# Kernel optimization log

Hardware: AMD Instinct MI355X
Metric: run time of the kernel (lower is better)

Reference implementation:

```python
import jax, jax.numpy as jnp
import numpy as np
import math

D_MODEL = 32
N_HEADS = 2
FEAT_DIM = 16
HEAD_DIM = 16  # d_model // num_key_value_heads
EPS = 1e-12
R2 = math.sqrt(2.0)
RD = math.sqrt(FEAT_DIM)
RRD = math.sqrt(RD)


def taylor_exp(x):
    # x: (b, h, l, f) -> (b, h, l, 1 + f + f*f)
    b, h, l, f = x.shape
    x2 = (x[..., :, None] * x[..., None, :]).reshape(b, h, l, f * f) / R2
    term1 = jnp.ones_like(x[..., :1])
    term2 = x / RRD
    term3 = x2 / RD
    return jnp.concatenate([term1, term2, term3], axis=-1)


def setup_inputs() -> dict:
    key = jax.random.key(0)
    ks = jax.random.split(key, 5)
    b, l = 4, 2048
    return {
        "hidden_states": jax.random.normal(ks[0], (b, l, D_MODEL), dtype=jnp.float32),
        "Wq": jax.random.normal(ks[1], (FEAT_DIM * N_HEADS, D_MODEL), dtype=jnp.float32) * (1.0 / math.sqrt(D_MODEL)),
        "Wk": jax.random.normal(ks[2], (FEAT_DIM * N_HEADS, D_MODEL), dtype=jnp.float32) * (1.0 / math.sqrt(D_MODEL)),
        "Wv": jax.random.normal(ks[3], (N_HEADS * HEAD_DIM, D_MODEL), dtype=jnp.float32) * (1.0 / math.sqrt(D_MODEL)),
        "Wo": jax.random.normal(ks[4], (D_MODEL, N_HEADS * HEAD_DIM), dtype=jnp.float32) * (1.0 / math.sqrt(D_MODEL)),
    }


def reference(hidden_states, Wq, Wk, Wv, Wo):
    b, l, _ = hidden_states.shape
    # projections (nn.Linear: x @ W.T)
    q = (hidden_states @ Wq.T).reshape(b, l, N_HEADS, FEAT_DIM).transpose(0, 2, 1, 3)  # (b,h,l,f)
    k = (hidden_states @ Wk.T).reshape(b, l, N_HEADS, FEAT_DIM).transpose(0, 2, 1, 3)
    v = (hidden_states @ Wv.T).reshape(b, l, N_HEADS, HEAD_DIM).transpose(0, 2, 1, 3)  # (b,h,l,d)

    q = taylor_exp(q)  # (b,h,l,D) with D = 1+f+f^2 = 273
    k = taylor_exp(k)

    # causal linear attention: num_t = q_t . sum_{s<=t} k_s v_s^T
    kv = jnp.cumsum(k[..., None, :] * v[..., :, None], axis=2)  # (b,h,l,d,D)
    num = jnp.einsum('bhlD,bhldD->bhld', q, kv)                  # (b,h,l,d)
    denom = jnp.einsum('bhlD,bhlD->bhl', q, jnp.cumsum(k, axis=2)) + EPS
    y = num / denom[..., None]

    y = y.transpose(0, 2, 1, 3).reshape(b, l, N_HEADS * HEAD_DIM)  # (b,l,h*d)
    return (y @ Wo.T).astype(hidden_states.dtype)
```

## Files before the change

kernel.cpp:

```cpp
#include <hip/hip_runtime.h>
#include <math.h>

#define B 4
#define H 2
#define L 2048
#define DM 32
#define F 16
#define HD 16
#define DD 273
#define CHK 64
#define NC (L / CHK)
#define BH (B * H)

#define SC_LIN 0.5f
#define SC_QUAD 0.17677669529663687f

__global__ __launch_bounds__(256) void proj_kernel(
    const float* __restrict__ hs, const float* __restrict__ Wq,
    const float* __restrict__ Wk, const float* __restrict__ Wv,
    float* __restrict__ qp, float* __restrict__ kp, float* __restrict__ vp) {
  int lane = threadIdx.x & 63;
  int wave = __builtin_amdgcn_readfirstlane(threadIdx.x >> 6);
  int rg = blockIdx.x >> 1;
  int half = blockIdx.x & 1;
  int row = rg * 64 + lane;
  int b = row >> 11, l = row & (L - 1);

  float x[DM];
  const float4* xr = (const float4*)(hs + (size_t)row * DM);
#pragma unroll
  for (int j = 0; j < DM / 4; j++) {
    float4 v = xr[j];
    x[4 * j] = v.x; x[4 * j + 1] = v.y; x[4 * j + 2] = v.z; x[4 * j + 3] = v.w;
  }
  int c0 = half * 48 + wave * 12;
  for (int c = c0; c < c0 + 12; c++) {
    int kind = c >> 5;
    int cc = c & 31;
    const float* __restrict__ W = (kind == 0) ? Wq : (kind == 1) ? Wk : Wv;
    const float* __restrict__ wr = W + (size_t)cc * DM;
    float acc = 0.f;
#pragma unroll
    for (int i = 0; i < DM; i++) acc += x[i] * wr[i];
    int h = cc >> 4, f = cc & 15;
    float* dst = (kind == 0) ? qp : (kind == 1) ? kp : vp;
    dst[(((size_t)(b * H + h) * L) + l) * F + f] = acc;
  }
}

__global__ __launch_bounds__(256) void chunksum_kernel(
    const float* __restrict__ kp, const float* __restrict__ vp,
    float* __restrict__ S_kv, float* __restrict__ S_k) {
  int blk = blockIdx.x;
  int bh = blk >> 5, ch = blk & (NC - 1);
  __shared__ float ks[CHK][F + 1];

  const float4* kb = (const float4*)(kp + ((size_t)bh * L + (size_t)ch * CHK) * F);
  {
    int r = threadIdx.x >> 2, c4 = (threadIdx.x & 3) * 4;
    float4 v = kb[threadIdx.x];
    ks[r][c4] = v.x; ks[r][c4 + 1] = v.y; ks[r][c4 + 2] = v.z; ks[r][c4 + 3] = v.w;
  }
  if (threadIdx.x < CHK) ks[threadIdx.x][16] = 1.0f;
  __syncthreads();

  const float* __restrict__ vbase = vp + ((size_t)bh * L + (size_t)ch * CHK) * F;

#pragma unroll
  for (int rep = 0; rep < 2; rep++) {
    int dd = threadIdx.x + rep * 256;
    if (dd >= DD) break;
    int i, j;
    float sc;
    if (dd == 0) {
      i = 16; j = 16; sc = 1.0f;
    } else if (dd <= F) {
      i = dd - 1; j = 16; sc = SC_LIN;
    } else {
      int m = dd - 17;
      i = m >> 4; j = m & 15; sc = SC_QUAD;
    }
    float acc[HD];
#pragma unroll
    for (int hh = 0; hh < HD; hh++) acc[hh] = 0.f;
    float acck = 0.f;
    for (int p = 0; p < CHK; p++) {
      float kf = sc * ks[p][i] * ks[p][j];
      acck += kf;
      const float* __restrict__ vr = vbase + p * F;
#pragma unroll
      for (int hh = 0; hh < HD; hh++) acc[hh] += kf * vr[hh];
    }
    float* dst = S_kv + ((size_t)blk * DD + dd) * HD;
#pragma unroll
    for (int hh = 0; hh < HD; hh++) dst[hh] = acc[hh];
    S_k[(size_t)blk * DD + dd] = acck;
  }
}

#define PSLICES 19
__global__ __launch_bounds__(256) void prefix_kernel(float* __restrict__ S_kv,
                                                     float* __restrict__ S_k) {
  int blk = blockIdx.x;
  int bh = blk / PSLICES, sl = blk % PSLICES;
  int e = sl * 256 + threadIdx.x;
  if (e < DD * HD) {
    size_t base = (size_t)bh * NC * DD * HD + e;
    float v[NC];
#pragma unroll
    for (int c = 0; c < NC; c++) v[c] = S_kv[base + (size_t)c * DD * HD];
    float run = 0.f;
#pragma unroll
    for (int c = 0; c < NC; c++) {
      S_kv[base + (size_t)c * DD * HD] = run;
      run += v[c];
    }
  } else if (e < DD * HD + DD) {
    int e2 = e - DD * HD;
    size_t base = (size_t)bh * NC * DD + e2;
    float v[NC];
#pragma unroll
    for (int c = 0; c < NC; c++) v[c] = S_k[base + (size_t)c * DD];
    float run = 0.f;
#pragma unroll
    for (int c = 0; c < NC; c++) {
      S_k[base + (size_t)c * DD] = run;
      run += v[c];
    }
  }
}

__global__ __launch_bounds__(512) void outchunk_kernel(
    const float* __restrict__ qp, const float* __restrict__ kp,
    const float* __restrict__ vp, const float* __restrict__ St_kv,
    const float* __restrict__ St_k, float* __restrict__ y) {
  int blk = blockIdx.x;
  int bh = blk >> 5, ch = blk & (NC - 1);
  int b = bh >> 1, h = bh & 1;
  int t = threadIdx.x & 63;
  int u = __builtin_amdgcn_readfirstlane(threadIdx.x >> 6);

  __shared__ float qs[CHK][F + 1];
  __shared__ float red[8][CHK][21];

  if (threadIdx.x < 256) {
    const float4* qb =
        (const float4*)(qp + ((size_t)bh * L + (size_t)ch * CHK) * F);
    int r = threadIdx.x >> 2, c4 = (threadIdx.x & 3) * 4;
    float4 v = qb[threadIdx.x];
    qs[r][c4] = v.x; qs[r][c4 + 1] = v.y; qs[r][c4 + 2] = v.z; qs[r][c4 + 3] = v.w;
    if (threadIdx.x < CHK) qs[threadIdx.x][16] = 1.0f;
  }

  float qreg[F];
  const float4* qrow =
      (const float4*)(qp + ((size_t)bh * L + (size_t)ch * CHK + t) * F);
#pragma unroll
  for (int j = 0; j < 4; j++) {
    float4 v = qrow[j];
    qreg[4 * j] = v.x; qreg[4 * j + 1] = v.y;
    qreg[4 * j + 2] = v.z; qreg[4 * j + 3] = v.w;
  }
  __syncthreads();

  float acc[HD];
#pragma unroll
  for (int hh = 0; hh < HD; hh++) acc[hh] = 0.f;
  float den = 0.f;

  const float* __restrict__ Sbase = St_kv + (size_t)blk * DD * HD;
  const float* __restrict__ Skb = St_k + (size_t)blk * DD;

  for (int m = 0; m < 35; m++) {
    int dd = u + (m << 3);
    if (dd >= DD) break;
    float phi;
    if (dd == 0) {
      phi = 1.0f;
    } else if (dd <= F) {
      phi = qs[t][dd - 1] * SC_LIN;
    } else {
      int mm = dd - 17;
      phi = qs[t][mm >> 4] * qs[t][mm & 15] * SC_QUAD;
    }
    den += phi * Skb[dd];
    const float* __restrict__ Sr = Sbase + dd * HD;
#pragma unroll
    for (int jj = 0; jj < HD; jj++) acc[jj] += phi * Sr[jj];
  }

  const float* __restrict__ kbase = kp + ((size_t)bh * L + (size_t)ch * CHK) * F;
  const float* __restrict__ vbase = vp + ((size_t)bh * L + (size_t)ch * CHK) * F;
#pragma unroll
  for (int mm = 0; mm < CHK / 8; mm++) {
    int s = u + mm * 8;
    const float* __restrict__ kr = kbase + s * F;
    float dot = 0.f;
#pragma unroll
    for (int i = 0; i < F; i++) dot += qreg[i] * kr[i];
    float scv = 1.0f + dot * 0.25f + dot * dot * 0.03125f;
    scv = (s <= t) ? scv : 0.0f;
    den += scv;
    const float* __restrict__ vr = vbase + s * F;
#pragma unroll
    for (int hh = 0; hh < HD; hh++) acc[hh] += scv * vr[hh];
  }

#pragma unroll
  for (int hh = 0; hh < HD; hh++) red[u][t][hh] = acc[hh];
  red[u][t][16] = den;
  __syncthreads();

  for (int idx = threadIdx.x; idx < CHK * 17; idx += 512) {
    int t2 = idx / 17, e = idx % 17;
    float sum = 0.f;
#pragma unroll
    for (int w = 0; w < 8; w++) sum += red[w][t2][e];
    red[0][t2][e] = sum;
  }
  __syncthreads();

  if (threadIdx.x < CHK) {
    int t2 = threadIdx.x;
    float inv = 1.0f / (red[0][t2][16] + 1e-12f);
    float* yb = y + (((size_t)(b * L + ch * CHK + t2)) * H + h) * HD;
#pragma unroll
    for (int hh = 0; hh < HD; hh++) yb[hh] = red[0][t2][hh] * inv;
  }
}

__global__ __launch_bounds__(256) void out_kernel(const float* __restrict__ y,
                                                  const float* __restrict__ Wo,
                                                  float* __restrict__ out) {
  int lane = threadIdx.x & 63;
  int wave = __builtin_amdgcn_readfirstlane(threadIdx.x >> 6);
  int row = blockIdx.x * 64 + lane;
  float yr[DM];
  const float4* yb = (const float4*)(y + (size_t)row * DM);
#pragma unroll
  for (int j = 0; j < DM / 4; j++) {
    float4 v = yb[j];
    yr[4 * j] = v.x; yr[4 * j + 1] = v.y; yr[4 * j + 2] = v.z; yr[4 * j + 3] = v.w;
  }
  for (int c = wave * 8; c < wave * 8 + 8; c++) {
    const float* __restrict__ wr = Wo + (size_t)c * DM;
    float acc = 0.f;
#pragma unroll
    for (int i = 0; i < DM; i++) acc += yr[i] * wr[i];
    out[(size_t)row * DM + c] = acc;
  }
}

extern "C" void kernel_launch(void* const* d_in, const int* in_sizes, int n_in,
                              void* d_out, int out_size, void* d_ws,
                              size_t ws_size, hipStream_t stream) {
  const float* hs = (const float*)d_in[0];
  const float* Wq = (const float*)d_in[1];
  const float* Wk = (const float*)d_in[2];
  const float* Wv = (const float*)d_in[3];
  const float* Wo = (const float*)d_in[4];
  float* out = (float*)d_out;

  float* ws = (float*)d_ws;
  float* qp = ws;
  float* kp = qp + (size_t)BH * L * F;
  float* vp = kp + (size_t)BH * L * F;
  float* S_kv = vp + (size_t)BH * L * F;
  float* S_k = S_kv + (size_t)BH * NC * DD * HD;
  float* y = S_k + (size_t)BH * NC * DD;

  proj_kernel<<<256, 256, 0, stream>>>(hs, Wq, Wk, Wv, qp, kp, vp);
  chunksum_kernel<<<BH * NC, 256, 0, stream>>>(kp, vp, S_kv, S_k);
  prefix_kernel<<<BH * PSLICES, 256, 0, stream>>>(S_kv, S_k);
  outchunk_kernel<<<BH * NC, 512, 0, stream>>>(qp, kp, vp, S_kv, S_k, y);
  out_kernel<<<B * L / 64, 256, 0, stream>>>(y, Wo, out);
}
```

Baseline: 106.5 us.

## Fuse QKV projection into chunk-sum kernel with fp16 LDS V and padded state

```diff
diff --git a/kernel.cpp b/kernel.cpp
--- a/kernel.cpp
+++ b/kernel.cpp
@@ -1,4 +1,5 @@
 #include <hip/hip_runtime.h>
+#include <hip/hip_fp16.h>
 #include <math.h>
 
 #define B 4
@@ -8,6 +9,7 @@
 #define F 16
 #define HD 16
 #define DD 273
+#define DDP 280
 #define CHK 64
 #define NC (L / CHK)
 #define BH (B * H)
@@ -15,61 +17,54 @@
 #define SC_LIN 0.5f
 #define SC_QUAD 0.17677669529663687f
 
-__global__ __launch_bounds__(256) void proj_kernel(
+__global__ __launch_bounds__(256) void chunksum_kernel(
     const float* __restrict__ hs, const float* __restrict__ Wq,
     const float* __restrict__ Wk, const float* __restrict__ Wv,
-    float* __restrict__ qp, float* __restrict__ kp, float* __restrict__ vp) {
-  int lane = threadIdx.x & 63;
-  int wave = __builtin_amdgcn_readfirstlane(threadIdx.x >> 6);
-  int rg = blockIdx.x >> 1;
-  int half = blockIdx.x & 1;
-  int row = rg * 64 + lane;
-  int b = row >> 11, l = row & (L - 1);
+    float* __restrict__ qp, float* __restrict__ kp, float* __restrict__ vp,
+    float* __restrict__ S_kv, float* __restrict__ S_k) {
+  int blk = blockIdx.x;
+  int bh = blk >> 5, ch = blk & (NC - 1);
+  int b = bh >> 1, h = bh & 1;
+  int lane = threadIdx.x & 63, wave = threadIdx.x >> 6;
+  int l = ch * CHK + lane;
+
+  __shared__ float ks[CHK][F + 1];
+  __shared__ __half vs_h[CHK][F];
 
   float x[DM];
-  const float4* xr = (const float4*)(hs + (size_t)row * DM);
+  const float4* xr = (const float4*)(hs + ((size_t)b * L + l) * DM);
 #pragma unroll
   for (int j = 0; j < DM / 4; j++) {
     float4 v = xr[j];
     x[4 * j] = v.x; x[4 * j + 1] = v.y; x[4 * j + 2] = v.z; x[4 * j + 3] = v.w;
   }
-  int c0 = half * 48 + wave * 12;
-  for (int c = c0; c < c0 + 12; c++) {
-    int kind = c >> 5;
-    int cc = c & 31;
+  for (int c = wave * 12; c < wave * 12 + 12; c++) {
+    int kind = c >> 4;
+    int f = c & 15;
     const float* __restrict__ W = (kind == 0) ? Wq : (kind == 1) ? Wk : Wv;
-    const float* __restrict__ wr = W + (size_t)cc * DM;
+    const float* wr = W + (size_t)(h * 16 + f) * DM;
     float acc = 0.f;
 #pragma unroll
     for (int i = 0; i < DM; i++) acc += x[i] * wr[i];
-    int h = cc >> 4, f = cc & 15;
     float* dst = (kind == 0) ? qp : (kind == 1) ? kp : vp;
-    dst[(((size_t)(b * H + h) * L) + l) * F + f] = acc;
-  }
-}
-
-__global__ __launch_bounds__(256) void chunksum_kernel(
-    const float* __restrict__ kp, const float* __restrict__ vp,
-    float* __restrict__ S_kv, float* __restrict__ S_k) {
-  int blk = blockIdx.x;
-  int bh = blk >> 5, ch = blk & (NC - 1);
-  __shared__ float ks[CHK][F + 1];
-
-  const float4* kb = (const float4*)(kp + ((size_t)bh * L + (size_t)ch * CHK) * F);
-  {
-    int r = threadIdx.x >> 2, c4 = (threadIdx.x & 3) * 4;
-    float4 v = kb[threadIdx.x];
-    ks[r][c4] = v.x; ks[r][c4 + 1] = v.y; ks[r][c4 + 2] = v.z; ks[r][c4 + 3] = v.w;
+    dst[((size_t)bh * L + l) * F + f] = acc;
+    if (kind == 1) ks[lane][f] = acc;
+    if (kind == 2) vs_h[lane][f] = __float2half(acc);
   }
   if (threadIdx.x < CHK) ks[threadIdx.x][16] = 1.0f;
   __syncthreads();
-
-  const float* __restrict__ vbase = vp + ((size_t)bh * L + (size_t)ch * CHK) * F;
 
 #pragma unroll
   for (int rep = 0; rep < 2; rep++) {
     int dd = threadIdx.x + rep * 256;
-    if (dd >= DD) break;
+    if (dd >= DDP) break;
+    float* dst = S_kv + ((size_t)blk * DDP + dd) * HD;
+    if (dd >= DD) {
+#pragma unroll
+      for (int hh = 0; hh < HD; hh++) dst[hh] = 0.f;
+      S_k[(size_t)blk * DDP + dd] = 0.f;
+      continue;
+    }
     int i, j;
     float sc;
     if (dd == 0) {
@@ -87,14 +82,17 @@
     for (int p = 0; p < CHK; p++) {
       float kf = sc * ks[p][i] * ks[p][j];
       acck += kf;
-      const float* __restrict__ vr = vbase + p * F;
-#pragma unroll
-      for (int hh = 0; hh < HD; hh++) acc[hh] += kf * vr[hh];
-    }
-    float* dst = S_kv + ((size_t)blk * DD + dd) * HD;
+      const __half2* vr = (const __half2*)vs_h[p];
+#pragma unroll
+      for (int x2 = 0; x2 < 8; x2++) {
+        float2 vf = __half22float2(vr[x2]);
+        acc[2 * x2] += kf * vf.x;
+        acc[2 * x2 + 1] += kf * vf.y;
+      }
+    }
 #pragma unroll
     for (int hh = 0; hh < HD; hh++) dst[hh] = acc[hh];
-    S_k[(size_t)blk * DD + dd] = acck;
+    S_k[(size_t)blk * DDP + dd] = acck;
   }
 }
 
@@ -104,27 +102,27 @@
   int blk = blockIdx.x;
   int bh = blk / PSLICES, sl = blk % PSLICES;
   int e = sl * 256 + threadIdx.x;
-  if (e < DD * HD) {
-    size_t base = (size_t)bh * NC * DD * HD + e;
+  if (e < DDP * HD) {
+    size_t base = (size_t)bh * NC * DDP * HD + e;
     float v[NC];
 #pragma unroll
-    for (int c = 0; c < NC; c++) v[c] = S_kv[base + (size_t)c * DD * HD];
+    for (int c = 0; c < NC; c++) v[c] = S_kv[base + (size_t)c * DDP * HD];
     float run = 0.f;
 #pragma unroll
     for (int c = 0; c < NC; c++) {
-      S_kv[base + (size_t)c * DD * HD] = run;
+      S_kv[base + (size_t)c * DDP * HD] = run;
       run += v[c];
     }
-  } else if (e < DD * HD + DD) {
-    int e2 = e - DD * HD;
-    size_t base = (size_t)bh * NC * DD + e2;
+  } else if (e < DDP * HD + DDP) {
+    int e2 = e - DDP * HD;
+    size_t base = (size_t)bh * NC * DDP + e2;
     float v[NC];
 #pragma unroll
-    for (int c = 0; c < NC; c++) v[c] = S_k[base + (size_t)c * DD];
+    for (int c = 0; c < NC; c++) v[c] = S_k[base + (size_t)c * DDP];
     float run = 0.f;
 #pragma unroll
     for (int c = 0; c < NC; c++) {
-      S_k[base + (size_t)c * DD] = run;
+      S_k[base + (size_t)c * DDP] = run;
       run += v[c];
     }
   }
@@ -168,12 +166,12 @@
   for (int hh = 0; hh < HD; hh++) acc[hh] = 0.f;
   float den = 0.f;
 
-  const float* __restrict__ Sbase = St_kv + (size_t)blk * DD * HD;
-  const float* __restrict__ Skb = St_k + (size_t)blk * DD;
-
+  const float* __restrict__ Sbase = St_kv + (size_t)blk * DDP * HD;
+  const float* __restrict__ Skb = St_k + (size_t)blk * DDP;
+
+#pragma unroll 5
   for (int m = 0; m < 35; m++) {
     int dd = u + (m << 3);
-    if (dd >= DD) break;
     float phi;
     if (dd == 0) {
       phi = 1.0f;
@@ -183,10 +181,18 @@
       int mm = dd - 17;
       phi = qs[t][mm >> 4] * qs[t][mm & 15] * SC_QUAD;
     }
+    phi = (dd < DD) ? phi : 0.0f;
     den += phi * Skb[dd];
-    const float* __restrict__ Sr = Sbase + dd * HD;
-#pragma unroll
-    for (int jj = 0; jj < HD; jj++) acc[jj] += phi * Sr[jj];
+    const float4* Sr = (const float4*)(Sbase + dd * HD);
+    float4 s0 = Sr[0], s1 = Sr[1], s2 = Sr[2], s3 = Sr[3];
+    acc[0] += phi * s0.x;  acc[1] += phi * s0.y;
+    acc[2] += phi * s0.z;  acc[3] += phi * s0.w;
+    acc[4] += phi * s1.x;  acc[5] += phi * s1.y;
+    acc[6] += phi * s1.z;  acc[7] += phi * s1.w;
+    acc[8] += phi * s2.x;  acc[9] += phi * s2.y;
+    acc[10] += phi * s2.z; acc[11] += phi * s2.w;
+    acc[12] += phi * s3.x; acc[13] += phi * s3.y;
+    acc[14] += phi * s3.z; acc[15] += phi * s3.w;
   }
 
   const float* __restrict__ kbase = kp + ((size_t)bh * L + (size_t)ch * CHK) * F;
@@ -194,16 +200,27 @@
 #pragma unroll
   for (int mm = 0; mm < CHK / 8; mm++) {
     int s = u + mm * 8;
-    const float* __restrict__ kr = kbase + s * F;
-    float dot = 0.f;
-#pragma unroll
-    for (int i = 0; i < F; i++) dot += qreg[i] * kr[i];
+    const float4* kr = (const float4*)(kbase + s * F);
+    float4 k0 = kr[0], k1 = kr[1], k2 = kr[2], k3 = kr[3];
+    float dot = qreg[0] * k0.x + qreg[1] * k0.y + qreg[2] * k0.z +
+                qreg[3] * k0.w + qreg[4] * k1.x + qreg[5] * k1.y +
+                qreg[6] * k1.z + qreg[7] * k1.w + qreg[8] * k2.x +
+                qreg[9] * k2.y + qreg[10] * k2.z + qreg[11] * k2.w +
+                qreg[12] * k3.x + qreg[13] * k3.y + qreg[14] * k3.z +
+                qreg[15] * k3.w;
     float scv = 1.0f + dot * 0.25f + dot * dot * 0.03125f;
     scv = (s <= t) ? scv : 0.0f;
     den += scv;
-    const float* __restrict__ vr = vbase + s * F;
-#pragma unroll
-    for (int hh = 0; hh < HD; hh++) acc[hh] += scv * vr[hh];
+    const float4* vr = (const float4*)(vbase + s * F);
+    float4 v0 = vr[0], v1 = vr[1], v2 = vr[2], v3 = vr[3];
+    acc[0] += scv * v0.x;  acc[1] += scv * v0.y;
+    acc[2] += scv * v0.z;  acc[3] += scv * v0.w;
+    acc[4] += scv * v1.x;  acc[5] += scv * v1.y;
+    acc[6] += scv * v1.z;  acc[7] += scv * v1.w;
+    acc[8] += scv * v2.x;  acc[9] += scv * v2.y;
+    acc[10] += scv * v2.z; acc[11] += scv * v2.w;
+    acc[12] += scv * v3.x; acc[13] += scv * v3.y;
+    acc[14] += scv * v3.z; acc[15] += scv * v3.w;
   }
 
 #pragma unroll
@@ -266,11 +283,11 @@
   float* kp = qp + (size_t)BH * L * F;
   float* vp = kp + (size_t)BH * L * F;
   float* S_kv = vp + (size_t)BH * L * F;
-  float* S_k = S_kv + (size_t)BH * NC * DD * HD;
-  float* y = S_k + (size_t)BH * NC * DD;
-
-  proj_kernel<<<256, 256, 0, stream>>>(hs, Wq, Wk, Wv, qp, kp, vp);
-  chunksum_kernel<<<BH * NC, 256, 0, stream>>>(kp, vp, S_kv, S_k);
+  float* S_k = S_kv + (size_t)BH * NC * DDP * HD;
+  float* y = S_k + (size_t)BH * NC * DDP;
+
+  chunksum_kernel<<<BH * NC, 256, 0, stream>>>(hs, Wq, Wk, Wv, qp, kp, vp,
+                                               S_kv, S_k);
   prefix_kernel<<<BH * PSLICES, 256, 0, stream>>>(S_kv, S_k);
   outchunk_kernel<<<BH * NC, 512, 0, stream>>>(qp, kp, vp, S_kv, S_k, y);
   out_kernel<<<B * L / 64, 256, 0, stream>>>(y, Wo, out);
```

Result: no change. 108.2 us (+1.6%).
